# Kernel optimization log

Hardware: AMD Instinct MI355X
Metric: run time of the kernel (lower is better)

The kernel has to match this reference:

```python
import jax, jax.numpy as jnp
import numpy as np

N = 100000      # nodes
E = 1600000     # edges (avg degree 16)
F_IN = 128      # num_features
H = 128         # hidden_channels
OUT = 64        # out_channels


def _glorot(key, shape):
    lim = float(np.sqrt(6.0 / (shape[0] + shape[1])))
    return jax.random.uniform(key, shape, jnp.float32, -lim, lim)


def setup_inputs() -> dict:
    key = jax.random.key(0)
    ks = jax.random.split(key, 5)
    x = jax.random.normal(ks[0], (N, F_IN), jnp.float32)
    edge_index = jax.random.randint(ks[1], (2, E), 0, N, dtype=jnp.int64)
    W1 = _glorot(ks[2], (F_IN, H)); b1 = jnp.zeros((H,), jnp.float32)
    W2 = _glorot(ks[3], (H, H));    b2 = jnp.zeros((H,), jnp.float32)
    W3 = _glorot(ks[4], (H, OUT));  b3 = jnp.zeros((OUT,), jnp.float32)
    return {"x": x, "edge_index": edge_index,
            "W1": W1, "b1": b1, "W2": W2, "b2": b2, "W3": W3, "b3": b3}


def _gcn_conv(h, src, dst, norm, W, b, n):
    # PyG GCNConv: linear transform, then sym-normalized scatter aggregation, then bias
    h = h @ W                                   # [N, d_out]
    msg = h[src] * norm[:, None]                # gather + scale, [E+N, d_out]
    agg = jax.ops.segment_sum(msg, dst, num_segments=n)
    return agg + b


def reference(x, edge_index, W1, b1, W2, b2, W3, b3):
    n = x.shape[0]
    # add self-loops (GCNConv default add_self_loops=True)
    loop = jnp.arange(n, dtype=edge_index.dtype)
    src = jnp.concatenate([edge_index[0], loop])
    dst = jnp.concatenate([edge_index[1], loop])
    # symmetric normalization deg^-1/2[src] * deg^-1/2[dst]
    deg = jax.ops.segment_sum(jnp.ones_like(dst, x.dtype), dst, num_segments=n)
    dinv = jnp.where(deg > 0, jax.lax.rsqrt(deg), 0.0)
    norm = dinv[src] * dinv[dst]

    h = jax.nn.relu(_gcn_conv(x, src, dst, norm, W1, b1, n))  # dropout p=0 -> no-op
    h = jax.nn.relu(_gcn_conv(h, src, dst, norm, W2, b2, n))
    h = _gcn_conv(h, src, dst, norm, W3, b3, n)
    return jax.nn.log_softmax(h, axis=1)
```

## Files before the change

kernel.cpp:

```cpp
#include <hip/hip_runtime.h>
#include <stdint.h>
#include <math.h>

#define FIN 128

typedef __attribute__((ext_vector_type(8))) short short8v;
typedef __attribute__((ext_vector_type(4))) float float4v;
typedef __attribute__((ext_vector_type(2))) float float2v;

__device__ __forceinline__ uint32_t f2_to_bf2(float x, float y) {
    uint32_t r;
    asm("v_cvt_pk_bf16_f32 %0, %1, %2" : "=v"(r) : "v"(x), "v"(y));
    return r;
}
__device__ __forceinline__ unsigned short f_to_bf(float x) {
    union { float f; uint32_t i; } a;
    a.f = x;
    uint32_t u = a.i + 0x7FFF + ((a.i >> 16) & 1);
    return (unsigned short)(u >> 16);
}
__device__ __forceinline__ void acc8_fp8_pk(float2v* acc2, uint2 v) {
    acc2[0] += __builtin_amdgcn_cvt_pk_f32_fp8(v.x, false);
    acc2[1] += __builtin_amdgcn_cvt_pk_f32_fp8(v.x, true);
    acc2[2] += __builtin_amdgcn_cvt_pk_f32_fp8(v.y, false);
    acc2[3] += __builtin_amdgcn_cvt_pk_f32_fp8(v.y, true);
}

template <int CTRL>
__device__ __forceinline__ float dppmov(float x) {
    int i = __builtin_bit_cast(int, x);
    int r = __builtin_amdgcn_update_dpp(i, i, CTRL, 0xF, 0xF, false);
    return __builtin_bit_cast(float, r);
}
__device__ __forceinline__ float swz16f(float x) {
    int r = __builtin_amdgcn_ds_swizzle(__builtin_bit_cast(int, x), 0x401F);
    return __builtin_bit_cast(float, r);
}

__device__ __forceinline__ int edge_at(const void* ei, long long idx, int is32) {
    return is32 ? ((const int*)ei)[idx] : (int)((const long long*)ei)[idx];
}

#define SP_CHUNK 4096
__global__ __launch_bounds__(256) void splitA_kernel(const void* __restrict__ ei,
                                                     int* __restrict__ gCnt,
                                                     uint32_t* __restrict__ buf1,
                                                     int E, int capS) {
    __shared__ int hist[16];
    __shared__ int gbase[16];
    __shared__ int lflag;
    int t = threadIdx.x;
    if (t < 16) hist[t] = 0;
    if (t == 0) lflag = 0;
    long long base = (long long)blockIdx.x * SP_CHUNK;
    __syncthreads();
    {
        long long e = base + t;
        if (e < E && ((const int*)ei)[2 * e + 1] != 0) atomicOr(&lflag, 1);
    }
    __syncthreads();
    int is32 = lflag;
    uint32_t lrec[16], rec[16];
#pragma unroll
    for (int j = 0; j < 16; ++j) {
        long long e = base + t + j * 256;
        if (e < E) {
            int s = edge_at(ei, e, is32);
            int d = edge_at(ei, (long long)E + e, is32);
            int b = d >> 13;
            int lofs = atomicAdd(&hist[b], 1);
            lrec[j] = ((uint32_t)lofs << 4) | (uint32_t)b;
            rec[j] = ((uint32_t)s << 13) | (uint32_t)(d & 8191);
        } else
            lrec[j] = 0xFFFFFFFFu;
    }
    __syncthreads();
    if (t < 16) gbase[t] = atomicAdd(&gCnt[t], hist[t]);
    __syncthreads();
#pragma unroll
    for (int j = 0; j < 16; ++j) {
        if (lrec[j] != 0xFFFFFFFFu) {
            int b = lrec[j] & 15;
            int pos = gbase[b] + (int)(lrec[j] >> 4);
            if (pos < capS) buf1[(size_t)b * capS + pos] = rec[j];
        }
    }
}

__global__ __launch_bounds__(256) void splitB_kernel(const int* __restrict__ gCnt,
                                                     const uint32_t* __restrict__ buf1,
                                                     int* __restrict__ cnt2,
                                                     uint32_t* __restrict__ buf2,
                                                     int capS, int cap2, int NB) {
    __shared__ int hist[128];
    __shared__ int gbase[128];
    int t = threadIdx.x;
    int s = blockIdx.y;
    if (t < 128) hist[t] = 0;
    __syncthreads();
    int m = gCnt[s];
    if (m > capS) m = capS;
    long long base = (long long)blockIdx.x * SP_CHUNK;
    uint32_t lrec[16], r32[16];
#pragma unroll
    for (int j = 0; j < 16; ++j) {
        long long i = base + t + j * 256;
        if (i < m) {
            uint32_t r = buf1[(size_t)s * capS + i];
            int d13 = (int)(r & 8191u);
            int sub = d13 >> 6;
            int lofs = atomicAdd(&hist[sub], 1);
            lrec[j] = ((uint32_t)lofs << 7) | (uint32_t)sub;
            r32[j] = ((r >> 13) << 6) | (uint32_t)(d13 & 63);
        } else
            lrec[j] = 0xFFFFFFFFu;
    }
    __syncthreads();
    if (t < 128) {
        int g = s * 128 + t;
        gbase[t] = (g < NB) ? atomicAdd(&cnt2[g], hist[t]) : 0;
    }
    __syncthreads();
#pragma unroll
    for (int j = 0; j < 16; ++j) {
        if (lrec[j] != 0xFFFFFFFFu) {
            int sub = lrec[j] & 127;
            int pos = gbase[sub] + (int)(lrec[j] >> 7);
            if (pos < cap2) buf2[(size_t)(s * 128 + sub) * cap2 + pos] = r32[j];
        }
    }
}

__global__ __launch_bounds__(256) void binBC_kernel(const int* __restrict__ cnt2,
                                                    const uint32_t* __restrict__ buf2,
                                                    int* __restrict__ cnt,
                                                    float* __restrict__ dinv,
                                                    int* __restrict__ rowstart,
                                                    int* __restrict__ col,
                                                    int n, int cap2) {
    __shared__ int h[64];
    __shared__ int rowst[64];
    __shared__ int cur[64];
    __shared__ int sc[64];
    int bin = blockIdx.x;
    int t = threadIdx.x;
    if (t < 64) {
        h[t] = (bin * 64 + t < n) ? 1 : 0;
        cur[t] = 1;
    }
    __syncthreads();
    int m = cnt2[bin];
    if (m > cap2) m = cap2;
    const uint32_t* buf = buf2 + (size_t)bin * cap2;
    for (int i = t; i < m; i += 256) atomicAdd(&h[buf[i] & 63], 1);
    __syncthreads();
    int c = 0, pc = 0;
    if (t < 64) { c = h[t]; pc = (c + 3) & ~3; sc[t] = pc; }
    __syncthreads();
    for (int off = 1; off < 64; off <<= 1) {
        int v = 0;
        if (t < 64 && t >= off) v = sc[t - off];
        __syncthreads();
        if (t < 64) sc[t] += v;
        __syncthreads();
    }
    if (t < 64) {
        int node = bin * 64 + t;
        int base = bin * cap2;
        int st = base + sc[t] - pc;
        rowst[t] = st;
        if (node < n) {
            cnt[node] = c;
            dinv[node] = rsqrtf((float)c);
            rowstart[node] = st;
            col[st] = node;
            for (int k = c; k < pc; ++k) col[st + k] = n;
        }
    }
    __syncthreads();
    for (int i = t; i < m; i += 256) {
        uint32_t rec = buf[i];
        int d6 = rec & 63;
        int off = atomicAdd(&cur[d6], 1);
        col[rowst[d6] + off] = (int)(rec >> 6);
    }
}

__global__ __launch_bounds__(256) void wconv_all(const float* __restrict__ W1,
                                                 const float* __restrict__ W2,
                                                 const float* __restrict__ W3,
                                                 unsigned short* __restrict__ Wf1,
                                                 unsigned short* __restrict__ Wf2,
                                                 unsigned short* __restrict__ Wf3) {
    int idx = blockIdx.x * 256 + threadIdx.x;
    const float* W;
    unsigned short* Wf;
    int NCOL, base;
    if (idx < 2048)      { W = W1; Wf = Wf1; NCOL = 128; base = idx; }
    else if (idx < 4096) { W = W2; Wf = Wf2; NCOL = 128; base = idx - 2048; }
    else if (idx < 5120) { W = W3; Wf = Wf3; NCOL = 64;  base = idx - 4096; }
    else return;
    int f = base >> 6, l = base & 63;
    int ct = f >> 2, ks = f & 3;
    int nn = ct * 16 + (l & 15);
    int k0 = ks * 32 + (l >> 4) * 8;
    uint32_t pk[4];
#pragma unroll
    for (int j = 0; j < 4; ++j) {
        float a = W[(size_t)(k0 + 2 * j) * NCOL + nn];
        float b = W[(size_t)(k0 + 2 * j + 1) * NCOL + nn];
        pk[j] = f2_to_bf2(a, b);
    }
    uint4 v = make_uint4(pk[0], pk[1], pk[2], pk[3]);
    ((uint4*)Wf)[base] = v;
}

template <int NCOL, int A_FP32, int OUT_FP8>
__global__ __launch_bounds__(256) void gemm_mfma(const void* __restrict__ Av,
                                                 const unsigned short* __restrict__ Wf,
                                                 const float* __restrict__ dinv,
                                                 void* __restrict__ Cv, int n) {
    __shared__ unsigned short lds[NCOL * 128];
    const int t = threadIdx.x;
    if (blockIdx.x == 0 && t < NCOL / 4)
        ((uint32_t*)Cv)[(size_t)n * (NCOL / 4) + t] = 0;
    for (int i = t; i < NCOL * 16; i += 256)
        ((uint4*)lds)[i] = ((const uint4*)Wf)[i];
    __syncthreads();

    const int wave = t >> 6, lane = t & 63;
    const int row0 = blockIdx.x * 64 + wave * 16;
    const int m = lane & 15, quad = lane >> 4;
    int arow = row0 + m;
    if (arow >= n) arow = n - 1;

    short8v a[4];
    if (A_FP32) {
        const float* A = (const float*)Av;
#pragma unroll
        for (int ks = 0; ks < 4; ++ks) {
            float4 lo = *(const float4*)(A + (size_t)arow * 128 + ks * 32 + quad * 8);
            float4 hi = *(const float4*)(A + (size_t)arow * 128 + ks * 32 + quad * 8 + 4);
            union { short8v v; uint32_t u[4]; } pk;
            pk.u[0] = f2_to_bf2(lo.x, lo.y);
            pk.u[1] = f2_to_bf2(lo.z, lo.w);
            pk.u[2] = f2_to_bf2(hi.x, hi.y);
            pk.u[3] = f2_to_bf2(hi.z, hi.w);
            a[ks] = pk.v;
        }
    } else {
        const unsigned short* A = (const unsigned short*)Av;
#pragma unroll
        for (int ks = 0; ks < 4; ++ks)
            a[ks] = *(const short8v*)(A + (size_t)arow * 128 + ks * 32 + quad * 8);
    }

    const int cr0 = row0 + quad * 4;
    float ds[4];
#pragma unroll
    for (int r = 0; r < 4; ++r) {
        int gr = cr0 + r;
        ds[r] = (gr < n) ? dinv[gr] : 0.0f;
    }
#pragma unroll
    for (int ct = 0; ct < NCOL / 16; ++ct) {
        float4v acc = {0.0f, 0.0f, 0.0f, 0.0f};
#pragma unroll
        for (int ks = 0; ks < 4; ++ks) {
            int f = ct * 4 + ks;
            short8v b = *(const short8v*)(lds + ((size_t)(f * 64 + lane)) * 8);
            acc = __builtin_amdgcn_mfma_f32_16x16x32_bf16(a[ks], b, acc, 0, 0, 0);
        }
#pragma unroll
        for (int r = 0; r < 4; ++r) {
            int gr = cr0 + r;
            if (gr < n) {
                float val = acc[r] * ds[r];
                if (OUT_FP8) {
                    int u = __builtin_amdgcn_cvt_pk_fp8_f32(val, val, 0, false);
                    ((unsigned char*)Cv)[(size_t)gr * NCOL + ct * 16 + m] =
                        (unsigned char)(u & 0xFF);
                } else {
                    ((unsigned short*)Cv)[(size_t)gr * NCOL + ct * 16 + m] = f_to_bf(val);
                }
            }
        }
    }
}

__global__ __launch_bounds__(256) void agg_relu_128_fp8(
        const uint32_t* __restrict__ T8, const int* __restrict__ rowstart,
        const int* __restrict__ cnt, const int* __restrict__ col,
        const float* __restrict__ dinv, const float* __restrict__ bias,
        uint32_t* __restrict__ outHb, int n) {
    int wid = blockIdx.x * 4 + (threadIdx.x >> 6);
    int lane = threadIdx.x & 63;
    int slot = lane & 1, j = (lane >> 1) & 15, sel = lane >> 5;
    int nodeA = wid * 2;
    int node = nodeA + sel;
    if (nodeA >= n) return;
    bool valid = node < n;
    int nd = valid ? node : nodeA;
    int start = rowstart[nd];
    int c = cnt[nd];
    int pend = start + ((c + 3) & ~3);
    if (!valid) pend = start;

    float2v acc2[4];
#pragma unroll
    for (int k = 0; k < 4; ++k) acc2[k] = (float2v){0.0f, 0.0f};
    const uint2* T2 = (const uint2*)T8;
    for (int p = start; p < pend; p += 4) {
        int s0 = col[p + slot];
        int s1 = col[p + slot + 2];
        uint2 v0 = T2[(size_t)s0 * 16 + j];
        uint2 v1 = T2[(size_t)s1 * 16 + j];
        acc8_fp8_pk(acc2, v0);
        acc8_fp8_pk(acc2, v1);
    }
    float* acc = (float*)acc2;
#pragma unroll
    for (int k = 0; k < 8; ++k) acc[k] += dppmov<0xB1>(acc[k]);
    float di = dinv[nd];
    const float4* b4 = (const float4*)bias;
    float4 bb0 = b4[j * 2], bb1 = b4[j * 2 + 1];
    float r[8];
    r[0] = fmaxf(di * acc[0] + bb0.x, 0.0f);
    r[1] = fmaxf(di * acc[1] + bb0.y, 0.0f);
    r[2] = fmaxf(di * acc[2] + bb0.z, 0.0f);
    r[3] = fmaxf(di * acc[3] + bb0.w, 0.0f);
    r[4] = fmaxf(di * acc[4] + bb1.x, 0.0f);
    r[5] = fmaxf(di * acc[5] + bb1.y, 0.0f);
    r[6] = fmaxf(di * acc[6] + bb1.z, 0.0f);
    r[7] = fmaxf(di * acc[7] + bb1.w, 0.0f);
    if (slot == 0 && valid) {
        uint4 o;
        o.x = f2_to_bf2(r[0], r[1]);
        o.y = f2_to_bf2(r[2], r[3]);
        o.z = f2_to_bf2(r[4], r[5]);
        o.w = f2_to_bf2(r[6], r[7]);
        *(uint4*)(outHb + (size_t)node * 64 + j * 4) = o;
    }
}

__global__ __launch_bounds__(256) void agg_lsm_64_fp8(
        const uint32_t* __restrict__ T8, const int* __restrict__ rowstart,
        const int* __restrict__ cnt, const int* __restrict__ col,
        const float* __restrict__ dinv, const float* __restrict__ bias,
        float* __restrict__ out, int n) {
    int wid = blockIdx.x * 4 + (threadIdx.x >> 6);
    int lane = threadIdx.x & 63;
    int slot = lane & 3, j = (lane >> 2) & 7, sel = lane >> 5;
    int nodeA = wid * 2;
    int node = nodeA + sel;
    if (nodeA >= n) return;
    bool valid = node < n;
    int nd = valid ? node : nodeA;
    int start = rowstart[nd];
    int c = cnt[nd];
    int pend = start + ((c + 3) & ~3);
    if (!valid) pend = start;

    float2v acc2[4];
#pragma unroll
    for (int k = 0; k < 4; ++k) acc2[k] = (float2v){0.0f, 0.0f};
    const uint2* T2 = (const uint2*)T8;
    for (int p = start; p < pend; p += 4) {
        int s0 = col[p + slot];
        uint2 v0 = T2[(size_t)s0 * 8 + j];
        acc8_fp8_pk(acc2, v0);
    }
    float* acc = (float*)acc2;
#pragma unroll
    for (int k = 0; k < 8; ++k) acc[k] += dppmov<0xB1>(acc[k]);
#pragma unroll
    for (int k = 0; k < 8; ++k) acc[k] += dppmov<0x4E>(acc[k]);
    float di = dinv[nd];
    const float4* b4 = (const float4*)bias;
    float4 bb0 = b4[j * 2], bb1 = b4[j * 2 + 1];
    float r[8];
    r[0] = di * acc[0] + bb0.x;
    r[1] = di * acc[1] + bb0.y;
    r[2] = di * acc[2] + bb0.z;
    r[3] = di * acc[3] + bb0.w;
    r[4] = di * acc[4] + bb1.x;
    r[5] = di * acc[5] + bb1.y;
    r[6] = di * acc[6] + bb1.z;
    r[7] = di * acc[7] + bb1.w;
    float m0 = fmaxf(fmaxf(r[0], r[1]), fmaxf(r[2], r[3]));
    float m1 = fmaxf(fmaxf(r[4], r[5]), fmaxf(r[6], r[7]));
    float m = fmaxf(m0, m1);
    m = fmaxf(m, dppmov<0x124>(m));
    m = fmaxf(m, dppmov<0x128>(m));
    m = fmaxf(m, swz16f(m));
    float e0 = __expf(r[0] - m) + __expf(r[1] - m);
    float e1 = __expf(r[2] - m) + __expf(r[3] - m);
    float e2 = __expf(r[4] - m) + __expf(r[5] - m);
    float e3 = __expf(r[6] - m) + __expf(r[7] - m);
    float ss = (e0 + e1) + (e2 + e3);
    ss += dppmov<0x124>(ss);
    ss += dppmov<0x128>(ss);
    ss += swz16f(ss);
    float lg = m + __logf(ss);
    if (slot == 0 && valid) {
        float4 o0 = make_float4(r[0] - lg, r[1] - lg, r[2] - lg, r[3] - lg);
        float4 o1 = make_float4(r[4] - lg, r[5] - lg, r[6] - lg, r[7] - lg);
        *(float4*)(out + (size_t)node * 64 + j * 8) = o0;
        *(float4*)(out + (size_t)node * 64 + j * 8 + 4) = o1;
    }
}

extern "C" void kernel_launch(void* const* d_in, const int* in_sizes, int n_in,
                              void* d_out, int out_size, void* d_ws, size_t ws_size,
                              hipStream_t stream) {
    const float* x  = (const float*)d_in[0];
    const void*  ei = d_in[1];
    const float* W1 = (const float*)d_in[2];
    const float* b1 = (const float*)d_in[3];
    const float* W2 = (const float*)d_in[4];
    const float* b2 = (const float*)d_in[5];
    const float* W3 = (const float*)d_in[6];
    const float* b3 = (const float*)d_in[7];
    float* out = (float*)d_out;

    const int n = in_sizes[0] / FIN;
    const int E = in_sizes[1] / 2;

    char* p = (char*)d_ws;
    auto carve = [&](size_t bytes) {
        char* q = p;
        p += (bytes + 255) & ~(size_t)255;
        return q;
    };
    const int NB = (n + 63) / 64;
    const int NS = (n + 8191) / 8192;

    long long meanS = (long long)E * 8192 / n;
    int capS = (int)(meanS + 8 * (long long)sqrt((double)meanS) + 1024);
    capS = (capS + 15) & ~15;
    long long mean2 = (long long)E * 64 / n;
    int cap2 = (int)(mean2 + 8 * (long long)sqrt((double)mean2) + 832);
    cap2 = (cap2 + 15) & ~15;

    int*   cnt      = (int*)carve((size_t)n * 4);
    int*   rowstart = (int*)carve((size_t)n * 4);
    float* dinv     = (float*)carve((size_t)n * 4);
    int*   colb     = (int*)carve(((size_t)NB * cap2 + 4096) * 4);
    int*   gCnt     = (int*)carve((size_t)(16 + NB) * 4);
    int*   cnt2     = gCnt + 16;
    size_t Tbytes = (size_t)n * 128 + 256;
    size_t Hbytes = (size_t)n * 128 * 2;
    char*  TH = carve(Tbytes + Hbytes);
    void*  T  = (void*)TH;
    unsigned short* Hb = (unsigned short*)(TH + Tbytes);
    unsigned short* Wf1 = (unsigned short*)carve(128 * 128 * 2);
    unsigned short* Wf2 = (unsigned short*)carve(128 * 128 * 2);
    unsigned short* Wf3 = (unsigned short*)carve(128 * 64 * 2);

    size_t buf1B = ((size_t)NS * capS * 4 + 255) & ~(size_t)255;
    uint32_t* buf1 = (uint32_t*)TH;
    uint32_t* buf2 = (uint32_t*)(TH + buf1B);
    size_t avail2 = (Tbytes + Hbytes > buf1B) ? (Tbytes + Hbytes - buf1B) : 0;
    size_t maxc2 = avail2 / ((size_t)NB * 4);
    if ((size_t)cap2 > maxc2) cap2 = (int)maxc2;

    hipMemsetAsync(gCnt, 0, (size_t)(16 + NB) * 4, stream);

    const int gagg2 = ((n + 1) / 2 + 3) / 4;
    const int ggemm = (n + 63) / 64;
    const int gsplitA = (E + SP_CHUNK - 1) / SP_CHUNK;
    const int gsplitBx = (capS + SP_CHUNK - 1) / SP_CHUNK;

    splitA_kernel<<<gsplitA, 256, 0, stream>>>(ei, gCnt, buf1, E, capS);
    splitB_kernel<<<dim3(gsplitBx, NS), 256, 0, stream>>>(gCnt, buf1, cnt2, buf2, capS,
                                                          cap2, NB);
    binBC_kernel<<<NB, 256, 0, stream>>>(cnt2, buf2, cnt, dinv, rowstart, colb, n,
                                         cap2);
    wconv_all<<<20, 256, 0, stream>>>(W1, W2, W3, Wf1, Wf2, Wf3);

    gemm_mfma<128, 1, 1><<<ggemm, 256, 0, stream>>>(x, Wf1, dinv, T, n);
    agg_relu_128_fp8<<<gagg2, 256, 0, stream>>>((const uint32_t*)T, rowstart, cnt,
                                                colb, dinv, b1, (uint32_t*)Hb, n);
    gemm_mfma<128, 0, 1><<<ggemm, 256, 0, stream>>>(Hb, Wf2, dinv, T, n);
    agg_relu_128_fp8<<<gagg2, 256, 0, stream>>>((const uint32_t*)T, rowstart, cnt,
                                                colb, dinv, b2, (uint32_t*)Hb, n);
    gemm_mfma<64, 0, 1><<<ggemm, 256, 0, stream>>>(Hb, Wf3, dinv, T, n);
    agg_lsm_64_fp8<<<gagg2, 256, 0, stream>>>((const uint32_t*)T, rowstart, cnt, colb,
                                              dinv, b3, out, n);
}
```

Measured before the change: 323.1 us.

## Widen fp8 gathers to 16 bytes and software-pipeline row loads in aggregation kernels

Both aggregation kernels now have each lane load 16 fp8 values (uint4) per neighbour row instead of 8, and the lane-to-edge mapping is changed so more edges are in flight per node. The gather loop is software-pipelined two iterations ahead: out-of-range indices are redirected to row n (a padding row) rather than guarded by branches. Cross-lane reductions grow to cover 16 accumulators per lane, and the softmax reduction steps are adjusted to the new lane layout. The aim is fewer, wider memory transactions and hidden gather latency, at the cost of more registers and extra reduction shuffles. It relies on row n of the transformed feature buffer existing and holding zeros.

```diff
diff --git a/kernel.cpp b/kernel.cpp
--- a/kernel.cpp
+++ b/kernel.cpp
@@ -19,11 +19,13 @@
     uint32_t u = a.i + 0x7FFF + ((a.i >> 16) & 1);
     return (unsigned short)(u >> 16);
 }
-__device__ __forceinline__ void acc8_fp8_pk(float2v* acc2, uint2 v) {
-    acc2[0] += __builtin_amdgcn_cvt_pk_f32_fp8(v.x, false);
-    acc2[1] += __builtin_amdgcn_cvt_pk_f32_fp8(v.x, true);
-    acc2[2] += __builtin_amdgcn_cvt_pk_f32_fp8(v.y, false);
-    acc2[3] += __builtin_amdgcn_cvt_pk_f32_fp8(v.y, true);
+__device__ __forceinline__ void acc16_fp8_pk(float2v* acc2, uint4 v) {
+    uint32_t us[4] = {v.x, v.y, v.z, v.w};
+#pragma unroll
+    for (int q = 0; q < 4; ++q) {
+        acc2[q * 2 + 0] += __builtin_amdgcn_cvt_pk_f32_fp8(us[q], false);
+        acc2[q * 2 + 1] += __builtin_amdgcn_cvt_pk_f32_fp8(us[q], true);
+    }
 }
 
 template <int CTRL>
@@ -295,61 +297,6 @@
         uint32_t* __restrict__ outHb, int n) {
     int wid = blockIdx.x * 4 + (threadIdx.x >> 6);
     int lane = threadIdx.x & 63;
-    int slot = lane & 1, j = (lane >> 1) & 15, sel = lane >> 5;
-    int nodeA = wid * 2;
-    int node = nodeA + sel;
-    if (nodeA >= n) return;
-    bool valid = node < n;
-    int nd = valid ? node : nodeA;
-    int start = rowstart[nd];
-    int c = cnt[nd];
-    int pend = start + ((c + 3) & ~3);
-    if (!valid) pend = start;
-
-    float2v acc2[4];
-#pragma unroll
-    for (int k = 0; k < 4; ++k) acc2[k] = (float2v){0.0f, 0.0f};
-    const uint2* T2 = (const uint2*)T8;
-    for (int p = start; p < pend; p += 4) {
-        int s0 = col[p + slot];
-        int s1 = col[p + slot + 2];
-        uint2 v0 = T2[(size_t)s0 * 16 + j];
-        uint2 v1 = T2[(size_t)s1 * 16 + j];
-        acc8_fp8_pk(acc2, v0);
-        acc8_fp8_pk(acc2, v1);
-    }
-    float* acc = (float*)acc2;
-#pragma unroll
-    for (int k = 0; k < 8; ++k) acc[k] += dppmov<0xB1>(acc[k]);
-    float di = dinv[nd];
-    const float4* b4 = (const float4*)bias;
-    float4 bb0 = b4[j * 2], bb1 = b4[j * 2 + 1];
-    float r[8];
-    r[0] = fmaxf(di * acc[0] + bb0.x, 0.0f);
-    r[1] = fmaxf(di * acc[1] + bb0.y, 0.0f);
-    r[2] = fmaxf(di * acc[2] + bb0.z, 0.0f);
-    r[3] = fmaxf(di * acc[3] + bb0.w, 0.0f);
-    r[4] = fmaxf(di * acc[4] + bb1.x, 0.0f);
-    r[5] = fmaxf(di * acc[5] + bb1.y, 0.0f);
-    r[6] = fmaxf(di * acc[6] + bb1.z, 0.0f);
-    r[7] = fmaxf(di * acc[7] + bb1.w, 0.0f);
-    if (slot == 0 && valid) {
-        uint4 o;
-        o.x = f2_to_bf2(r[0], r[1]);
-        o.y = f2_to_bf2(r[2], r[3]);
-        o.z = f2_to_bf2(r[4], r[5]);
-        o.w = f2_to_bf2(r[6], r[7]);
-        *(uint4*)(outHb + (size_t)node * 64 + j * 4) = o;
-    }
-}
-
-__global__ __launch_bounds__(256) void agg_lsm_64_fp8(
-        const uint32_t* __restrict__ T8, const int* __restrict__ rowstart,
-        const int* __restrict__ cnt, const int* __restrict__ col,
-        const float* __restrict__ dinv, const float* __restrict__ bias,
-        float* __restrict__ out, int n) {
-    int wid = blockIdx.x * 4 + (threadIdx.x >> 6);
-    int lane = threadIdx.x & 63;
     int slot = lane & 3, j = (lane >> 2) & 7, sel = lane >> 5;
     int nodeA = wid * 2;
     int node = nodeA + sel;
@@ -358,55 +305,139 @@
     int nd = valid ? node : nodeA;
     int start = rowstart[nd];
     int c = cnt[nd];
-    int pend = start + ((c + 3) & ~3);
-    if (!valid) pend = start;
-
-    float2v acc2[4];
-#pragma unroll
-    for (int k = 0; k < 4; ++k) acc2[k] = (float2v){0.0f, 0.0f};
-    const uint2* T2 = (const uint2*)T8;
-    for (int p = start; p < pend; p += 4) {
-        int s0 = col[p + slot];
-        uint2 v0 = T2[(size_t)s0 * 8 + j];
-        acc8_fp8_pk(acc2, v0);
+    int nit = valid ? (((c + 3) & ~3) >> 2) : 0;
+
+    float2v acc2[8];
+#pragma unroll
+    for (int k = 0; k < 8; ++k) acc2[k] = (float2v){0.0f, 0.0f};
+    const uint4* T4 = (const uint4*)T8;
+    int bp = start + slot;
+    int s0 = col[bp];
+    s0 = (0 < nit) ? s0 : n;
+    uint4 vN = T4[(size_t)s0 * 8 + j];
+    int s1 = col[bp + 4];
+    s1 = (1 < nit) ? s1 : n;
+    uint4 vM = T4[(size_t)s1 * 8 + j];
+    for (int it = 0; it < nit; ++it) {
+        int s2 = col[bp + (it + 2) * 4];
+        s2 = (it + 2 < nit) ? s2 : n;
+        uint4 vP = T4[(size_t)s2 * 8 + j];
+        acc16_fp8_pk(acc2, vN);
+        vN = vM;
+        vM = vP;
     }
     float* acc = (float*)acc2;
 #pragma unroll
-    for (int k = 0; k < 8; ++k) acc[k] += dppmov<0xB1>(acc[k]);
-#pragma unroll
-    for (int k = 0; k < 8; ++k) acc[k] += dppmov<0x4E>(acc[k]);
+    for (int k = 0; k < 16; ++k) acc[k] += dppmov<0xB1>(acc[k]);
+#pragma unroll
+    for (int k = 0; k < 16; ++k) acc[k] += dppmov<0x4E>(acc[k]);
+    if (slot == 0 && valid) {
+        float di = dinv[node];
+        const float4* b4 = (const float4*)bias;
+        float r[16];
+#pragma unroll
+        for (int q = 0; q < 4; ++q) {
+            float4 bb = b4[j * 4 + q];
+            r[q * 4 + 0] = fmaxf(di * acc[q * 4 + 0] + bb.x, 0.0f);
+            r[q * 4 + 1] = fmaxf(di * acc[q * 4 + 1] + bb.y, 0.0f);
+            r[q * 4 + 2] = fmaxf(di * acc[q * 4 + 2] + bb.z, 0.0f);
+            r[q * 4 + 3] = fmaxf(di * acc[q * 4 + 3] + bb.w, 0.0f);
+        }
+        uint4 o0, o1;
+        o0.x = f2_to_bf2(r[0], r[1]);   o0.y = f2_to_bf2(r[2], r[3]);
+        o0.z = f2_to_bf2(r[4], r[5]);   o0.w = f2_to_bf2(r[6], r[7]);
+        o1.x = f2_to_bf2(r[8], r[9]);   o1.y = f2_to_bf2(r[10], r[11]);
+        o1.z = f2_to_bf2(r[12], r[13]); o1.w = f2_to_bf2(r[14], r[15]);
+        *(uint4*)(outHb + (size_t)node * 64 + j * 8) = o0;
+        *(uint4*)(outHb + (size_t)node * 64 + j * 8 + 4) = o1;
+    }
+}
+
+__global__ __launch_bounds__(256) void agg_lsm_64_fp8(
+        const uint32_t* __restrict__ T8, const int* __restrict__ rowstart,
+        const int* __restrict__ cnt, const int* __restrict__ col,
+        const float* __restrict__ dinv, const float* __restrict__ bias,
+        float* __restrict__ out, int n) {
+    int wid = blockIdx.x * 4 + (threadIdx.x >> 6);
+    int lane = threadIdx.x & 63;
+    int slot = (lane & 3) + ((lane >> 4) & 1) * 4;
+    int j = (lane >> 2) & 3, sel = lane >> 5;
+    int nodeA = wid * 2;
+    int node = nodeA + sel;
+    if (nodeA >= n) return;
+    bool valid = node < n;
+    int nd = valid ? node : nodeA;
+    int start = rowstart[nd];
+    int c = cnt[nd];
+    int pend = valid ? (start + ((c + 3) & ~3)) : start;
+    int nit = valid ? (((c + 3) & ~3) + 7) >> 3 : 0;
+
+    float2v acc2[8];
+#pragma unroll
+    for (int k = 0; k < 8; ++k) acc2[k] = (float2v){0.0f, 0.0f};
+    const uint4* T4 = (const uint4*)T8;
+    int bp = start + slot;
+    int i0 = bp;
+    int s0 = col[i0];
+    s0 = (i0 < pend) ? s0 : n;
+    uint4 vN = T4[(size_t)s0 * 4 + j];
+    int i1 = bp + 8;
+    int s1 = col[i1];
+    s1 = (i1 < pend) ? s1 : n;
+    uint4 vM = T4[(size_t)s1 * 4 + j];
+    for (int it = 0; it < nit; ++it) {
+        int i2 = bp + (it + 2) * 8;
+        int s2 = col[i2];
+        s2 = (i2 < pend) ? s2 : n;
+        uint4 vP = T4[(size_t)s2 * 4 + j];
+        acc16_fp8_pk(acc2, vN);
+        vN = vM;
+        vM = vP;
+    }
+    float* acc = (float*)acc2;
+#pragma unroll
+    for (int k = 0; k < 16; ++k) acc[k] += dppmov<0xB1>(acc[k]);
+#pragma unroll
+    for (int k = 0; k < 16; ++k) acc[k] += dppmov<0x4E>(acc[k]);
+#pragma unroll
+    for (int k = 0; k < 16; ++k) acc[k] += swz16f(acc[k]);
     float di = dinv[nd];
     const float4* b4 = (const float4*)bias;
-    float4 bb0 = b4[j * 2], bb1 = b4[j * 2 + 1];
-    float r[8];
-    r[0] = di * acc[0] + bb0.x;
-    r[1] = di * acc[1] + bb0.y;
-    r[2] = di * acc[2] + bb0.z;
-    r[3] = di * acc[3] + bb0.w;
-    r[4] = di * acc[4] + bb1.x;
-    r[5] = di * acc[5] + bb1.y;
-    r[6] = di * acc[6] + bb1.z;
-    r[7] = di * acc[7] + bb1.w;
+    float r[16];
+#pragma unroll
+    for (int q = 0; q < 4; ++q) {
+        float4 bb = b4[j * 4 + q];
+        r[q * 4 + 0] = di * acc[q * 4 + 0] + bb.x;
+        r[q * 4 + 1] = di * acc[q * 4 + 1] + bb.y;
+        r[q * 4 + 2] = di * acc[q * 4 + 2] + bb.z;
+        r[q * 4 + 3] = di * acc[q * 4 + 3] + bb.w;
+    }
     float m0 = fmaxf(fmaxf(r[0], r[1]), fmaxf(r[2], r[3]));
     float m1 = fmaxf(fmaxf(r[4], r[5]), fmaxf(r[6], r[7]));
-    float m = fmaxf(m0, m1);
+    float m2 = fmaxf(fmaxf(r[8], r[9]), fmaxf(r[10], r[11]));
+    float m3 = fmaxf(fmaxf(r[12], r[13]), fmaxf(r[14], r[15]));
+    float m = fmaxf(fmaxf(m0, m1), fmaxf(m2, m3));
     m = fmaxf(m, dppmov<0x124>(m));
     m = fmaxf(m, dppmov<0x128>(m));
-    m = fmaxf(m, swz16f(m));
-    float e0 = __expf(r[0] - m) + __expf(r[1] - m);
-    float e1 = __expf(r[2] - m) + __expf(r[3] - m);
-    float e2 = __expf(r[4] - m) + __expf(r[5] - m);
-    float e3 = __expf(r[6] - m) + __expf(r[7] - m);
+    float e0 = __expf(r[0] - m) + __expf(r[1] - m) + __expf(r[2] - m) +
+               __expf(r[3] - m);
+    float e1 = __expf(r[4] - m) + __expf(r[5] - m) + __expf(r[6] - m) +
+               __expf(r[7] - m);
+    float e2 = __expf(r[8] - m) + __expf(r[9] - m) + __expf(r[10] - m) +
+               __expf(r[11] - m);
+    float e3 = __expf(r[12] - m) + __expf(r[13] - m) + __expf(r[14] - m) +
+               __expf(r[15] - m);
     float ss = (e0 + e1) + (e2 + e3);
     ss += dppmov<0x124>(ss);
     ss += dppmov<0x128>(ss);
-    ss += swz16f(ss);
     float lg = m + __logf(ss);
     if (slot == 0 && valid) {
-        float4 o0 = make_float4(r[0] - lg, r[1] - lg, r[2] - lg, r[3] - lg);
-        float4 o1 = make_float4(r[4] - lg, r[5] - lg, r[6] - lg, r[7] - lg);
-        *(float4*)(out + (size_t)node * 64 + j * 8) = o0;
-        *(float4*)(out + (size_t)node * 64 + j * 8 + 4) = o1;
+#pragma unroll
+        for (int q = 0; q < 4; ++q) {
+            float4 o = make_float4(r[q * 4 + 0] - lg, r[q * 4 + 1] - lg,
+                                   r[q * 4 + 2] - lg, r[q * 4 + 3] - lg);
+            *(float4*)(out + (size_t)node * 64 + j * 16 + q * 4) = o;
+        }
     }
 }
 
```

Result: faster. 305.8 us (-5.4%).
